# Kernel optimization log

Measured on AMD Instinct MI355X. Metric: run time of the kernel, lower is better.

Reference implementation:

```python
import jax, jax.numpy as jnp
import numpy as np

B, S, D, H = 4, 1024, 1024, 16
DK = D // H
MASK_WEIGHT_0 = 1.0   # weight for key-type 0 (from (weight, mask_mat) tuple)
MASK_WEIGHT_1 = 0.5   # weight for key-type 1
NEG_INF = -1.0e9


def setup_inputs() -> dict:
    key = jax.random.key(0)
    ks = jax.random.split(key, 10)
    wscale = 0.02
    return {
        "query": jax.random.normal(ks[0], (B, S, D), jnp.float32),
        "key_x": jax.random.normal(ks[1], (B, S, D), jnp.float32),
        "value": jax.random.normal(ks[2], (B, S, D), jnp.float32),
        "mask0": jax.random.randint(ks[3], (B, S, S), 0, 2, jnp.int32),
        "mask1": jax.random.randint(ks[4], (B, S, S), 0, 2, jnp.int32),
        "Wq":  wscale * jax.random.normal(ks[5], (D, D), jnp.float32),
        "Wk0": wscale * jax.random.normal(ks[6], (D, D), jnp.float32),
        "Wk1": wscale * jax.random.normal(ks[7], (D, D), jnp.float32),
        "Wv":  wscale * jax.random.normal(ks[8], (D, D), jnp.float32),
        "Wo":  wscale * jax.random.normal(ks[9], (D, D), jnp.float32),
    }


def _heads(x, W):
    # torch nn.Linear: x @ W.T ; then view(B,S,H,DK).transpose(1,2)
    return (x @ W.T).reshape(B, S, H, DK).transpose(0, 2, 1, 3)  # [B,H,S,DK]


def reference(query, key_x, value, mask0, mask1, Wq, Wk0, Wk1, Wv, Wo):
    q = _heads(query, Wq)          # [B,H,S,DK]
    k0 = _heads(key_x, Wk0)
    k1 = _heads(key_x, Wk1)
    v = _heads(value, Wv)
    scale = 1.0 / jnp.sqrt(jnp.float32(DK))

    def masked_score(k, mask, weight):
        s = jnp.einsum('bhqd,bhkd->bhqk', q, k) * scale       # [B,H,S,S]
        keep = (mask != 0)[:, None, :, :]                     # broadcast over heads
        # (score * weight*keep).masked_fill(mask==0, -1e9)
        return jnp.where(keep, s * weight, NEG_INF)

    scores = masked_score(k0, mask0, MASK_WEIGHT_0) + masked_score(k1, mask1, MASK_WEIGHT_1)
    p_attn = jax.nn.sigmoid(scores)                           # activation='sigmoid'
    x = jnp.einsum('bhqk,bhkd->bhqd', p_attn, v)              # [B,H,S,DK]
    x = x.transpose(0, 2, 1, 3).reshape(B, S, D)
    return x @ Wo.T                                            # output_linear (dropout p=0)
```

## Files before the change

### kernel.cpp

```cpp
#include <hip/hip_runtime.h>

#define B_  4
#define S_  1024
#define D_  1024
#define H_  16
#define DK_ 64

typedef __attribute__((ext_vector_type(8)))  short bf16x8;
typedef __attribute__((ext_vector_type(4)))  short bf16x4;
typedef __attribute__((ext_vector_type(4)))  float f32x4;
typedef __attribute__((ext_vector_type(16))) float f32x16;

static __device__ __forceinline__ unsigned short f2bf(float f) {
  union { float f; unsigned u; } v; v.f = f;
  unsigned r = v.u + 0x7FFFu + ((v.u >> 16) & 1u);
  return (unsigned short)(r >> 16);
}

static __device__ __forceinline__ unsigned cvtpk(float lo, float hi) {
  unsigned r;
  asm("v_cvt_pk_bf16_f32 %0, %1, %2" : "=v"(r) : "v"(lo), "v"(hi));
  return r;
}
static __device__ __forceinline__ void plswap(unsigned &a, unsigned &b) {
  asm volatile("v_permlane32_swap_b32 %0, %1" : "+v"(a), "+v"(b));
}

typedef __attribute__((address_space(1))) const void gc_t;
typedef __attribute__((address_space(3))) void lds_t;
static __device__ __forceinline__ void gload_lds16(const void* g, void* l) {
  __builtin_amdgcn_global_load_lds((gc_t*)g, (lds_t*)l, 16, 0, 0);
}

#define TM_ (1u << 22)
#define WM_ (1u << 20)

#define CEXP_ (-0.18033688011112042f)

__global__ __launch_bounds__(256)
void cvt_w(const float* __restrict__ w0, const float* __restrict__ w1,
           const float* __restrict__ w2, const float* __restrict__ w3,
           const float* __restrict__ w4, unsigned short* __restrict__ wbf)
{
  const size_t u = ((size_t)blockIdx.x * 256 + threadIdx.x) * 8;
  const int seg = (int)(u >> 20);
  const size_t off = u & (WM_ - 1);
  unsigned short t[8];
  if (seg == 1) {
    float4 a0 = *(const float4*)(w1 + off);
    float4 a1 = *(const float4*)(w1 + off + 4);
    float4 b0 = *(const float4*)(w2 + off);
    float4 b1 = *(const float4*)(w2 + off + 4);
    t[0]=f2bf(a0.x+0.5f*b0.x); t[1]=f2bf(a0.y+0.5f*b0.y);
    t[2]=f2bf(a0.z+0.5f*b0.z); t[3]=f2bf(a0.w+0.5f*b0.w);
    t[4]=f2bf(a1.x+0.5f*b1.x); t[5]=f2bf(a1.y+0.5f*b1.y);
    t[6]=f2bf(a1.z+0.5f*b1.z); t[7]=f2bf(a1.w+0.5f*b1.w);
  } else {
    const float sc = (seg == 0) ? CEXP_ : 1.0f;
    const float* src = (seg == 0) ? w0 : (seg == 2 ? w3 : w4);
    float4 f0 = *(const float4*)(src + off);
    float4 f1 = *(const float4*)(src + off + 4);
    t[0]=f2bf(sc*f0.x); t[1]=f2bf(sc*f0.y);
    t[2]=f2bf(sc*f0.z); t[3]=f2bf(sc*f0.w);
    t[4]=f2bf(sc*f1.x); t[5]=f2bf(sc*f1.y);
    t[6]=f2bf(sc*f1.z); t[7]=f2bf(sc*f1.w);
  }
  *(bf16x8*)(wbf + (size_t)seg * WM_ + off) = *(bf16x8*)t;
}

__global__ __launch_bounds__(512, 6)
void proj_gemm(const float* __restrict__ qx, const float* __restrict__ kx,
               const float* __restrict__ vx,
               const unsigned short* __restrict__ wbf,
               unsigned short* __restrict__ Qb, unsigned short* __restrict__ Kh,
               unsigned short* __restrict__ Vth,
               const int* __restrict__ ma, const int* __restrict__ mb,
               unsigned long long* __restrict__ pk)
{
  __shared__ unsigned short As[128][64];
  __shared__ unsigned short Ws[128][64];

  const int tid = threadIdx.x, bid = blockIdx.x;

  if (bid >= 768) {
    const int row = (bid - 768) * 2 + (tid >> 8);
    const int w4  = (tid >> 6) & 3, lw = tid & 63;
    const int4 a  = *(const int4*)(ma + (size_t)row*1024 + w4*256 + lw*4);
    const int4 b  = *(const int4*)(mb + (size_t)row*1024 + w4*256 + lw*4);
    const unsigned long long b0 = __ballot((a.x != 0) & (b.x != 0));
    const unsigned long long b1 = __ballot((a.y != 0) & (b.y != 0));
    const unsigned long long b2 = __ballot((a.z != 0) & (b.z != 0));
    const unsigned long long b3 = __ballot((a.w != 0) & (b.w != 0));
    if (lw < 4) {
      const unsigned long long wv =
            ((b0 >> (16*lw)) & 0xFFFFull)
         | (((b1 >> (16*lw)) & 0xFFFFull) << 16)
         | (((b2 >> (16*lw)) & 0xFFFFull) << 32)
         | (((b3 >> (16*lw)) & 0xFFFFull) << 48);
      pk[(size_t)row*16 + w4*4 + lw] = wv;
    }
    return;
  }

  const int xcd = bid & 7, c = bid >> 3;
  const int L = xcd * 96 + c;
  const int which = L >> 8;
  const int rem = L & 255;
  const int mt = rem >> 3, nt = rem & 7;
  const int m0 = mt * 128, n0 = nt * 128;
  const int w = tid >> 6, l = tid & 63;
  const int lr = l & 15, lg = l >> 4;
  const int wr = w >> 1, wc = w & 1;

  const float* Af = (which == 0) ? qx : (which == 1) ? kx : vx;
  const unsigned short* W = wbf + (size_t)which * WM_;

  const f32x4 fzero = {0.f, 0.f, 0.f, 0.f};
  f32x4 acc[2][4];
#pragma unroll
  for (int m = 0; m < 2; m++)
#pragma unroll
    for (int n = 0; n < 4; n++) acc[m][n] = fzero;

  const int r0  = tid >> 3;
  const int cg  = tid & 7;
  const int aswz = (cg ^ (r0 & 7)) * 8;
  const float* aSrc = Af + (size_t)(m0 + r0) * 1024 + cg * 8;

  const int srow8 = l >> 3;
  const int sg    = ((l & 7) ^ srow8) * 8;
  const unsigned short* wBase = W + (size_t)(n0 + w*16 + srow8) * 1024 + sg;

  const int rc0 = ((lg)     ^ (lr & 7)) * 8;
  const int rc1 = ((4 + lg) ^ (lr & 7)) * 8;

  for (int kk = 0; kk < 1024; kk += 64) {
    float4 fa[2][2];
#pragma unroll
    for (int p = 0; p < 2; ++p) {
      const float* s = aSrc + (size_t)(p*64) * 1024 + kk;
      fa[p][0] = *(const float4*)s;
      fa[p][1] = *(const float4*)(s + 4);
    }
#pragma unroll
    for (int cc = 0; cc < 2; ++cc)
      gload_lds16(wBase + (size_t)cc * 8 * 1024 + kk, &Ws[w*16 + cc*8][0]);
#pragma unroll
    for (int p = 0; p < 2; ++p) {
      union { unsigned u[4]; bf16x8 v; } pu;
      pu.u[0] = cvtpk(fa[p][0].x, fa[p][0].y);
      pu.u[1] = cvtpk(fa[p][0].z, fa[p][0].w);
      pu.u[2] = cvtpk(fa[p][1].x, fa[p][1].y);
      pu.u[3] = cvtpk(fa[p][1].z, fa[p][1].w);
      *(bf16x8*)&As[p*64 + r0][aswz] = pu.v;
    }
    __syncthreads();

#pragma unroll
    for (int ks = 0; ks < 2; ++ks) {
      const int rc = ks ? rc1 : rc0;
      bf16x8 af[2], bfr[4];
#pragma unroll
      for (int m = 0; m < 2; m++) af[m]  = *(const bf16x8*)&As[wr*32 + m*16 + lr][rc];
#pragma unroll
      for (int n = 0; n < 4; n++) bfr[n] = *(const bf16x8*)&Ws[wc*64 + n*16 + lr][rc];
#pragma unroll
      for (int m = 0; m < 2; m++)
#pragma unroll
        for (int n = 0; n < 4; n++)
          acc[m][n] = __builtin_amdgcn_mfma_f32_16x16x32_bf16(af[m], bfr[n], acc[m][n], 0, 0, 0);
    }
    __syncthreads();
  }

  if (which == 2) {
#pragma unroll
    for (int m = 0; m < 2; m++) {
      const int row = m0 + wr*32 + m*16 + lg*4;
      const int b = row >> 10, s = row & 1023;
#pragma unroll
      for (int n = 0; n < 4; n++) {
        const int col = n0 + wc*64 + n*16 + lr;
        const int h = col >> 6, dk = col & 63;
        unsigned short tv[4] = {f2bf(acc[m][n][0]), f2bf(acc[m][n][1]),
                                f2bf(acc[m][n][2]), f2bf(acc[m][n][3])};
        const size_t a = ((size_t)((b*H_ + h)*DK_ + dk)) * S_
                       + (size_t)(s & ~63) + ((((s >> 3) & 7) ^ (dk & 7)) << 3) + (s & 7);
        *(bf16x4*)(Vth + a) = *(bf16x4*)tv;
      }
    }
  } else if (which == 0) {
#pragma unroll
    for (int m = 0; m < 2; m++) {
      const int row = m0 + wr*32 + m*16 + lg*4;
#pragma unroll
      for (int n = 0; n < 4; n++) {
        const int col = n0 + wc*64 + n*16 + lr;
#pragma unroll
        for (int r = 0; r < 4; r++)
          Qb[(size_t)(row + r) * 1024 + col] = f2bf(acc[m][n][r]);
      }
    }
  } else {
#pragma unroll
    for (int m = 0; m < 2; m++) {
      const int row = m0 + wr*32 + m*16 + lg*4;
#pragma unroll
      for (int n = 0; n < 4; n++) {
        const int col = n0 + wc*64 + n*16 + lr;
        const int h = col >> 6, dk = col & 63;
#pragma unroll
        for (int r = 0; r < 4; r++) {
          const int rr = row + r;
          const int b = rr >> 10, s = rr & 1023;
          const size_t a = ((size_t)((b*H_ + h)*S_ + s)) * 64
                         + (((dk >> 3) ^ (s & 7)) << 3) + (dk & 7);
          Kh[a] = f2bf(acc[m][n][r]);
        }
      }
    }
  }
}

__global__ __launch_bounds__(256, 4)
void out_gemm(const unsigned short* __restrict__ A,
              const unsigned short* __restrict__ W, float* __restrict__ C)
{
  __shared__ unsigned short As[128][64];
  __shared__ unsigned short Ws2[64][64];

  const int tid = threadIdx.x, bid = blockIdx.x;
  const int xcd = bid & 7, idx = bid >> 3;
  const int mt = (xcd << 2) | (idx & 3);
  const int nt = idx >> 2;
  const int m0 = mt * 128, n0 = nt * 64;
  const int w = tid >> 6, l = tid & 63;
  const int lr = l & 15, lg = l >> 4;
  const int wr = w >> 1, wc = w & 1;

  const f32x4 fzero = {0.f, 0.f, 0.f, 0.f};
  f32x4 acc[4][2];
#pragma unroll
  for (int m = 0; m < 4; m++)
#pragma unroll
    for (int n = 0; n < 2; n++) acc[m][n] = fzero;

  const int srow8 = l >> 3;
  const int sg    = ((l & 7) ^ srow8) * 8;
  const int rc0 = ((lg)     ^ (lr & 7)) * 8;
  const int rc1 = ((4 + lg) ^ (lr & 7)) * 8;

  const unsigned short* aBase = A + (size_t)(m0 + w*32 + srow8) * 1024 + sg;
  const unsigned short* wBase = W + (size_t)(n0 + w*16 + srow8) * 1024 + sg;

  for (int kk = 0; kk < 1024; kk += 64) {
#pragma unroll
    for (int cc = 0; cc < 4; ++cc)
      gload_lds16(aBase + (size_t)cc * 8 * 1024 + kk, &As[w*32 + cc*8][0]);
#pragma unroll
    for (int cc = 0; cc < 2; ++cc)
      gload_lds16(wBase + (size_t)cc * 8 * 1024 + kk, &Ws2[w*16 + cc*8][0]);
    __syncthreads();

#pragma unroll
    for (int ks = 0; ks < 2; ++ks) {
      const int rc = ks ? rc1 : rc0;
      bf16x8 af[4], bfr[2];
#pragma unroll
      for (int m = 0; m < 4; m++) af[m]  = *(const bf16x8*)&As[wr*64 + m*16 + lr][rc];
#pragma unroll
      for (int n = 0; n < 2; n++) bfr[n] = *(const bf16x8*)&Ws2[wc*32 + n*16 + lr][rc];
#pragma unroll
      for (int m = 0; m < 4; m++)
#pragma unroll
        for (int n = 0; n < 2; n++)
          acc[m][n] = __builtin_amdgcn_mfma_f32_16x16x32_bf16(af[m], bfr[n], acc[m][n], 0, 0, 0);
    }
    __syncthreads();
  }

#pragma unroll
  for (int m = 0; m < 4; m++) {
    const int row = m0 + wr*64 + m*16 + lg*4;
#pragma unroll
    for (int n = 0; n < 2; n++) {
      const int col = n0 + wc*32 + n*16 + lr;
#pragma unroll
      for (int r = 0; r < 4; r++)
        C[(size_t)(row + r) * 1024 + col] = acc[m][n][r];
    }
  }
}

__global__ __launch_bounds__(512)
void attn_kernel(const unsigned short* __restrict__ Q,
                 const unsigned short* __restrict__ Kh,
                 const unsigned short* __restrict__ Vth,
                 const unsigned long long* __restrict__ mpk,
                 unsigned short* __restrict__ X)
{
  __shared__ unsigned short Ks[2][2][4096];
  __shared__ unsigned short Vs[2][2][4096];

  const int tid  = threadIdx.x;
  const int bid0 = blockIdx.x;
  const int bid = ((bid0 & 7) << 6) | (bid0 >> 3);
  const int qt = bid & 7, h = (bid >> 3) & 15, b = bid >> 7;
  const int q0 = qt * 128;
  const int w8 = tid >> 6, lw = tid & 63;
  const int grp = w8 >> 2, qw = w8 & 3;
  const int l31 = lw & 31, hh = lw >> 5, l7 = lw & 7;
  const int bh = b * H_ + h;

  bf16x8 qf[4];
  {
    const unsigned short* qp = Q + ((size_t)(b*S_ + q0 + qw*32 + l31)) * D_ + h*DK_ + hh*8;
#pragma unroll
    for (int ds = 0; ds < 4; ++ds) qf[ds] = *(const bf16x8*)(qp + ds*16);
  }
  const size_t mbase = ((size_t)(b*S_ + q0 + qw*32 + l31)) * 16 + grp*8;

  f32x16 acc0, acc1;
#pragma unroll
  for (int r = 0; r < 16; ++r) { acc0[r] = 0.f; acc1[r] = 0.f; }

  const unsigned short* gp[4];
  unsigned short* lb[4];
  int stp[4];
#pragma unroll
  for (int c = 0; c < 4; ++c) {
    const int e = qw*4 + c;
    const int bu = e >> 3, s = e & 7;
    lb[c] = (bu == 0 ? &Ks[grp][0][0] : &Vs[grp][0][0]) + s*512;
    if (bu == 0) {
      gp[c]  = Kh + (size_t)bh * 65536 + grp*32768 + s*512 + lw*8;
      stp[c] = 4096;
    } else {
      gp[c]  = Vth + ((size_t)(bh*DK_ + s*8 + (lw >> 3))) * S_ + grp*512 + (lw & 7) * 8;
      stp[c] = 64;
    }
  }

#define STAGE(nxt)                                                     \
  {                                                                    \
    _Pragma("unroll")                                                  \
    for (int c = 0; c < 4; ++c) {                                      \
      gload_lds16(gp[c], lb[c] + (nxt)*4096);                          \
      gp[c] += stp[c];                                                 \
    }                                                                  \
  }

  STAGE(0);
  __syncthreads();
  unsigned long long mw = mpk[mbase];
  int cur = 0;

  for (int t = 0; t < 8; ++t) {
    unsigned long long mw_n = 0;
    if (t < 7) { STAGE(cur ^ 1); mw_n = mpk[mbase + t + 1]; }

#pragma unroll
    for (int sub = 0; sub < 2; ++sub) {
      const int rbase = (sub*32 + l31) * 64;
      f32x16 sv;
#pragma unroll
      for (int r = 0; r < 16; ++r) sv[r] = 0.f;
      __builtin_amdgcn_s_setprio(1);
#pragma unroll
      for (int ds = 0; ds < 4; ++ds) {
        const int g = (((ds*2 + hh) ^ l7)) * 8;
        const bf16x8 kf = *(const bf16x8*)&Ks[grp][cur][rbase + g];
        sv = __builtin_amdgcn_mfma_f32_32x32x16_bf16(kf, qf[ds], sv, 0, 0, 0);
      }
      __builtin_amdgcn_s_setprio(0);

      const unsigned long long ams = mw >> (8*sub + hh);
      float p[16];
#pragma unroll
      for (int r = 0; r < 16; ++r) {
        const int cbit = 16*(r & 3) + 2*(r >> 2);
        const float e  = __builtin_amdgcn_exp2f(sv[r]);
        const float pr = __builtin_amdgcn_rcpf(1.0f + e);
        p[r] = ((ams >> cbit) & 1ull) ? pr : 0.f;
      }

      bf16x8 pa[2];
#pragma unroll
      for (int ks = 0; ks < 2; ++ks) {
        const int a0 = ks*8;
        unsigned u0 = cvtpk(p[a0+0], p[a0+1]);
        unsigned u1 = cvtpk(p[a0+2], p[a0+3]);
        unsigned u2 = cvtpk(p[a0+4], p[a0+5]);
        unsigned u3 = cvtpk(p[a0+6], p[a0+7]);
        plswap(u0, u2);
        plswap(u1, u3);
        union { unsigned u[4]; bf16x8 v; } pu;
        pu.u[0] = u0; pu.u[1] = u1; pu.u[2] = u2; pu.u[3] = u3;
        pa[ks] = pu.v;
      }

      __builtin_amdgcn_s_setprio(1);
#pragma unroll
      for (int ks = 0; ks < 2; ++ks) {
        const int g = ((sub*4 + ks*2 + hh) ^ l7) * 8;
        const bf16x8 vb0 = *(const bf16x8*)&Vs[grp][cur][(l31)      * 64 + g];
        const bf16x8 vb1 = *(const bf16x8*)&Vs[grp][cur][(32 + l31) * 64 + g];
        acc0 = __builtin_amdgcn_mfma_f32_32x32x16_bf16(pa[ks], vb0, acc0, 0, 0, 0);
        acc1 = __builtin_amdgcn_mfma_f32_32x32x16_bf16(pa[ks], vb1, acc1, 0, 0, 0);
      }
      __builtin_amdgcn_s_setprio(0);
    }

    if (t < 7) {
      __syncthreads();
      mw = mw_n;
      cur ^= 1;
    }
  }
#undef STAGE

  __syncthreads();
  float2* cmb = (float2*)&Ks[0][0][0];
  if (grp == 1) {
#pragma unroll
    for (int i = 0; i < 8; ++i)
      cmb[(qw*16 + i)*64 + lw] = make_float2(acc0[2*i], acc0[2*i+1]);
#pragma unroll
    for (int i = 0; i < 8; ++i)
      cmb[(qw*16 + 8 + i)*64 + lw] = make_float2(acc1[2*i], acc1[2*i+1]);
  }
  __syncthreads();
  if (grp == 0) {
#pragma unroll
    for (int i = 0; i < 8; ++i) {
      float2 v = cmb[(qw*16 + i)*64 + lw];
      acc0[2*i] += v.x; acc0[2*i+1] += v.y;
    }
#pragma unroll
    for (int i = 0; i < 8; ++i) {
      float2 v = cmb[(qw*16 + 8 + i)*64 + lw];
      acc1[2*i] += v.x; acc1[2*i+1] += v.y;
    }
#pragma unroll
    for (int r = 0; r < 16; ++r) {
      const int qrow = q0 + qw*32 + (r & 3) + 8*(r >> 2) + 4*hh;
      unsigned short* xp = X + ((size_t)(b*S_ + qrow)) * D_ + h*DK_ + l31;
      xp[0]  = f2bf(acc0[r]);
      xp[32] = f2bf(acc1[r]);
    }
  }
}

extern "C" void kernel_launch(void* const* d_in, const int* in_sizes, int n_in,
                              void* d_out, int out_size, void* d_ws, size_t ws_size,
                              hipStream_t stream)
{
  const float* query = (const float*)d_in[0];
  const float* key_x = (const float*)d_in[1];
  const float* value = (const float*)d_in[2];
  const int*   mask0 = (const int*)d_in[3];
  const int*   mask1 = (const int*)d_in[4];
  const float* Wq    = (const float*)d_in[5];
  const float* Wk0   = (const float*)d_in[6];
  const float* Wk1   = (const float*)d_in[7];
  const float* Wv    = (const float*)d_in[8];
  const float* Wo    = (const float*)d_in[9];

  unsigned short* ws = (unsigned short*)d_ws;
  unsigned short* wbf = ws;
  unsigned short* Qb  = ws + (size_t)4 * WM_;
  unsigned short* Kh  = Qb  + (size_t)TM_;
  unsigned short* Vth = Kh  + (size_t)TM_;
  unsigned long long* mpk = (unsigned long long*)(Vth + (size_t)TM_);
  unsigned short* Xb = (unsigned short*)(mpk + 65536);

  cvt_w<<<dim3(2048), dim3(256), 0, stream>>>(Wq, Wk0, Wk1, Wv, Wo, wbf);

  proj_gemm<<<dim3(768 + 2048), dim3(512), 0, stream>>>(
      query, key_x, value, wbf, Qb, Kh, Vth, mask0, mask1, mpk);

  attn_kernel<<<dim3(B_ * H_ * (S_ / 128)), dim3(512), 0, stream>>>(
      Qb, Kh, Vth, mpk, Xb);

  out_gemm<<<dim3(512), dim3(256), 0, stream>>>(Xb, wbf + (size_t)3 * WM_,
                                                (float*)d_out);
}
```

Before: 93.41 us.

## Fuse weight fp32-to-bf16 conversion into projection and output GEMMs

Removes the separate cvt_w launch that pre-converted all five weight matrices to bf16. Weights are now loaded as fp32 and converted in registers before the LDS store inside proj_gemm and out_gemm, with the Wk0+0.5*Wk1 combine and the Q scale applied on the fly. This saves one kernel launch plus the write and re-read of the bf16 weight buffer. The cost is twice the global bytes per weight tile and repeated conversion in every tile that reuses a weight. The K path also reads two weight matrices per tile and replaces the async global_load_lds with a register path.

```diff
diff --git a/kernel.cpp b/kernel.cpp
--- a/kernel.cpp
+++ b/kernel.cpp
@@ -33,45 +33,14 @@
 }
 
 #define TM_ (1u << 22)
-#define WM_ (1u << 20)
 
 #define CEXP_ (-0.18033688011112042f)
-
-__global__ __launch_bounds__(256)
-void cvt_w(const float* __restrict__ w0, const float* __restrict__ w1,
-           const float* __restrict__ w2, const float* __restrict__ w3,
-           const float* __restrict__ w4, unsigned short* __restrict__ wbf)
-{
-  const size_t u = ((size_t)blockIdx.x * 256 + threadIdx.x) * 8;
-  const int seg = (int)(u >> 20);
-  const size_t off = u & (WM_ - 1);
-  unsigned short t[8];
-  if (seg == 1) {
-    float4 a0 = *(const float4*)(w1 + off);
-    float4 a1 = *(const float4*)(w1 + off + 4);
-    float4 b0 = *(const float4*)(w2 + off);
-    float4 b1 = *(const float4*)(w2 + off + 4);
-    t[0]=f2bf(a0.x+0.5f*b0.x); t[1]=f2bf(a0.y+0.5f*b0.y);
-    t[2]=f2bf(a0.z+0.5f*b0.z); t[3]=f2bf(a0.w+0.5f*b0.w);
-    t[4]=f2bf(a1.x+0.5f*b1.x); t[5]=f2bf(a1.y+0.5f*b1.y);
-    t[6]=f2bf(a1.z+0.5f*b1.z); t[7]=f2bf(a1.w+0.5f*b1.w);
-  } else {
-    const float sc = (seg == 0) ? CEXP_ : 1.0f;
-    const float* src = (seg == 0) ? w0 : (seg == 2 ? w3 : w4);
-    float4 f0 = *(const float4*)(src + off);
-    float4 f1 = *(const float4*)(src + off + 4);
-    t[0]=f2bf(sc*f0.x); t[1]=f2bf(sc*f0.y);
-    t[2]=f2bf(sc*f0.z); t[3]=f2bf(sc*f0.w);
-    t[4]=f2bf(sc*f1.x); t[5]=f2bf(sc*f1.y);
-    t[6]=f2bf(sc*f1.z); t[7]=f2bf(sc*f1.w);
-  }
-  *(bf16x8*)(wbf + (size_t)seg * WM_ + off) = *(bf16x8*)t;
-}
 
 __global__ __launch_bounds__(512, 6)
 void proj_gemm(const float* __restrict__ qx, const float* __restrict__ kx,
                const float* __restrict__ vx,
-               const unsigned short* __restrict__ wbf,
+               const float* __restrict__ w0, const float* __restrict__ w1,
+               const float* __restrict__ w2, const float* __restrict__ w3,
                unsigned short* __restrict__ Qb, unsigned short* __restrict__ Kh,
                unsigned short* __restrict__ Vth,
                const int* __restrict__ ma, const int* __restrict__ mb,
@@ -113,7 +82,7 @@
   const int wr = w >> 1, wc = w & 1;
 
   const float* Af = (which == 0) ? qx : (which == 1) ? kx : vx;
-  const unsigned short* W = wbf + (size_t)which * WM_;
+  const float* Wf = (which == 0) ? w0 : (which == 1) ? w1 : w3;
 
   const f32x4 fzero = {0.f, 0.f, 0.f, 0.f};
   f32x4 acc[2][4];
@@ -125,34 +94,57 @@
   const int r0  = tid >> 3;
   const int cg  = tid & 7;
   const int aswz = (cg ^ (r0 & 7)) * 8;
-  const float* aSrc = Af + (size_t)(m0 + r0) * 1024 + cg * 8;
-
-  const int srow8 = l >> 3;
-  const int sg    = ((l & 7) ^ srow8) * 8;
-  const unsigned short* wBase = W + (size_t)(n0 + w*16 + srow8) * 1024 + sg;
+  const float* aSrc  = Af + (size_t)(m0 + r0) * 1024 + cg * 8;
+  const float* wSrc  = Wf + (size_t)(n0 + r0) * 1024 + cg * 8;
+  const float* wSrc2 = w2 + (size_t)(n0 + r0) * 1024 + cg * 8;
 
   const int rc0 = ((lg)     ^ (lr & 7)) * 8;
   const int rc1 = ((4 + lg) ^ (lr & 7)) * 8;
 
   for (int kk = 0; kk < 1024; kk += 64) {
-    float4 fa[2][2];
+    float4 fa[2][2], fw[2][2], fw2[2][2];
 #pragma unroll
     for (int p = 0; p < 2; ++p) {
       const float* s = aSrc + (size_t)(p*64) * 1024 + kk;
       fa[p][0] = *(const float4*)s;
       fa[p][1] = *(const float4*)(s + 4);
-    }
-#pragma unroll
-    for (int cc = 0; cc < 2; ++cc)
-      gload_lds16(wBase + (size_t)cc * 8 * 1024 + kk, &Ws[w*16 + cc*8][0]);
+      const float* t = wSrc + (size_t)(p*64) * 1024 + kk;
+      fw[p][0] = *(const float4*)t;
+      fw[p][1] = *(const float4*)(t + 4);
+    }
+    if (which == 1) {
+#pragma unroll
+      for (int p = 0; p < 2; ++p) {
+        const float* t = wSrc2 + (size_t)(p*64) * 1024 + kk;
+        fw2[p][0] = *(const float4*)t;
+        fw2[p][1] = *(const float4*)(t + 4);
+      }
+    }
 #pragma unroll
     for (int p = 0; p < 2; ++p) {
-      union { unsigned u[4]; bf16x8 v; } pu;
-      pu.u[0] = cvtpk(fa[p][0].x, fa[p][0].y);
-      pu.u[1] = cvtpk(fa[p][0].z, fa[p][0].w);
-      pu.u[2] = cvtpk(fa[p][1].x, fa[p][1].y);
-      pu.u[3] = cvtpk(fa[p][1].z, fa[p][1].w);
-      *(bf16x8*)&As[p*64 + r0][aswz] = pu.v;
+      union { unsigned u[4]; bf16x8 v; } pa_, pw_;
+      pa_.u[0] = cvtpk(fa[p][0].x, fa[p][0].y);
+      pa_.u[1] = cvtpk(fa[p][0].z, fa[p][0].w);
+      pa_.u[2] = cvtpk(fa[p][1].x, fa[p][1].y);
+      pa_.u[3] = cvtpk(fa[p][1].z, fa[p][1].w);
+      *(bf16x8*)&As[p*64 + r0][aswz] = pa_.v;
+      if (which == 1) {
+        pw_.u[0] = cvtpk(fw[p][0].x + 0.5f*fw2[p][0].x, fw[p][0].y + 0.5f*fw2[p][0].y);
+        pw_.u[1] = cvtpk(fw[p][0].z + 0.5f*fw2[p][0].z, fw[p][0].w + 0.5f*fw2[p][0].w);
+        pw_.u[2] = cvtpk(fw[p][1].x + 0.5f*fw2[p][1].x, fw[p][1].y + 0.5f*fw2[p][1].y);
+        pw_.u[3] = cvtpk(fw[p][1].z + 0.5f*fw2[p][1].z, fw[p][1].w + 0.5f*fw2[p][1].w);
+      } else if (which == 0) {
+        pw_.u[0] = cvtpk(CEXP_*fw[p][0].x, CEXP_*fw[p][0].y);
+        pw_.u[1] = cvtpk(CEXP_*fw[p][0].z, CEXP_*fw[p][0].w);
+        pw_.u[2] = cvtpk(CEXP_*fw[p][1].x, CEXP_*fw[p][1].y);
+        pw_.u[3] = cvtpk(CEXP_*fw[p][1].z, CEXP_*fw[p][1].w);
+      } else {
+        pw_.u[0] = cvtpk(fw[p][0].x, fw[p][0].y);
+        pw_.u[1] = cvtpk(fw[p][0].z, fw[p][0].w);
+        pw_.u[2] = cvtpk(fw[p][1].x, fw[p][1].y);
+        pw_.u[3] = cvtpk(fw[p][1].z, fw[p][1].w);
+      }
+      *(bf16x8*)&Ws[p*64 + r0][aswz] = pw_.v;
     }
     __syncthreads();
 
@@ -224,7 +216,7 @@
 
 __global__ __launch_bounds__(256, 4)
 void out_gemm(const unsigned short* __restrict__ A,
-              const unsigned short* __restrict__ W, float* __restrict__ C)
+              const float* __restrict__ Wo, float* __restrict__ C)
 {
   __shared__ unsigned short As[128][64];
   __shared__ unsigned short Ws2[64][64];
@@ -251,15 +243,31 @@
   const int rc1 = ((4 + lg) ^ (lr & 7)) * 8;
 
   const unsigned short* aBase = A + (size_t)(m0 + w*32 + srow8) * 1024 + sg;
-  const unsigned short* wBase = W + (size_t)(n0 + w*16 + srow8) * 1024 + sg;
+
+  const int r0w = tid >> 2;
+  const int gp0 = (tid & 3) * 2;
+  const float* wSrc = Wo + (size_t)(n0 + r0w) * 1024 + gp0 * 8;
+  const int wz0 = (gp0       ^ (r0w & 7)) * 8;
+  const int wz1 = ((gp0 + 1) ^ (r0w & 7)) * 8;
 
   for (int kk = 0; kk < 1024; kk += 64) {
 #pragma unroll
     for (int cc = 0; cc < 4; ++cc)
       gload_lds16(aBase + (size_t)cc * 8 * 1024 + kk, &As[w*32 + cc*8][0]);
-#pragma unroll
-    for (int cc = 0; cc < 2; ++cc)
-      gload_lds16(wBase + (size_t)cc * 8 * 1024 + kk, &Ws2[w*16 + cc*8][0]);
+    {
+      const float* s = wSrc + kk;
+      float4 f0 = *(const float4*)s;
+      float4 f1 = *(const float4*)(s + 4);
+      float4 f2 = *(const float4*)(s + 8);
+      float4 f3 = *(const float4*)(s + 12);
+      union { unsigned u[4]; bf16x8 v; } p0_, p1_;
+      p0_.u[0] = cvtpk(f0.x, f0.y); p0_.u[1] = cvtpk(f0.z, f0.w);
+      p0_.u[2] = cvtpk(f1.x, f1.y); p0_.u[3] = cvtpk(f1.z, f1.w);
+      p1_.u[0] = cvtpk(f2.x, f2.y); p1_.u[1] = cvtpk(f2.z, f2.w);
+      p1_.u[2] = cvtpk(f3.x, f3.y); p1_.u[3] = cvtpk(f3.z, f3.w);
+      *(bf16x8*)&Ws2[r0w][wz0] = p0_.v;
+      *(bf16x8*)&Ws2[r0w][wz1] = p1_.v;
+    }
     __syncthreads();
 
 #pragma unroll
@@ -467,21 +475,17 @@
   const float* Wo    = (const float*)d_in[9];
 
   unsigned short* ws = (unsigned short*)d_ws;
-  unsigned short* wbf = ws;
-  unsigned short* Qb  = ws + (size_t)4 * WM_;
+  unsigned short* Qb  = ws;
   unsigned short* Kh  = Qb  + (size_t)TM_;
   unsigned short* Vth = Kh  + (size_t)TM_;
   unsigned long long* mpk = (unsigned long long*)(Vth + (size_t)TM_);
   unsigned short* Xb = (unsigned short*)(mpk + 65536);
 
-  cvt_w<<<dim3(2048), dim3(256), 0, stream>>>(Wq, Wk0, Wk1, Wv, Wo, wbf);
-
   proj_gemm<<<dim3(768 + 2048), dim3(512), 0, stream>>>(
-      query, key_x, value, wbf, Qb, Kh, Vth, mask0, mask1, mpk);
+      query, key_x, value, Wq, Wk0, Wk1, Wv, Qb, Kh, Vth, mask0, mask1, mpk);
 
   attn_kernel<<<dim3(B_ * H_ * (S_ / 128)), dim3(512), 0, stream>>>(
       Qb, Kh, Vth, mpk, Xb);
 
-  out_gemm<<<dim3(512), dim3(256), 0, stream>>>(Xb, wbf + (size_t)3 * WM_,
-                                                (float*)d_out);
-}
+  out_gemm<<<dim3(512), dim3(256), 0, stream>>>(Xb, Wo, (float*)d_out);
+}
```

After: 248.8 us. 2.66x slower.
